# Performance work log

Hardware: AMD Instinct MI355X
Metric: run time of the kernel (lower is better)

Reference implementation:

```python
import jax, jax.numpy as jnp
import numpy as np

B, N, K, UP = 8, 2048, 20, 2
CIN, D, COUT, PH, AH = 256, 64, 128, 64, 256
EPS = 1e-5

def c1(x, W, b):
    # 1x1 Conv1d: x (B,C,N), W (O,C)
    return jnp.einsum('oc,bcn->bon', W, x) + b[None, :, None]

def c2(x, W, b):
    # 1x1 Conv2d: x (B,C,N,K), W (O,C)
    return jnp.einsum('oc,bcnk->bonk', W, x) + b[None, :, None, None]

def bn2(x, g, be):
    # eval-mode BatchNorm2d with running_mean=0, running_var=1
    inv = np.float32(1.0 / np.sqrt(1.0 + EPS))
    return g[None, :, None, None] * x * inv + be[None, :, None, None]

def knn_idx(p, k):
    # p: (B,N,3) -> (B,N,k) indices of k nearest neighbors (incl. self)
    sq = jnp.sum(p * p, -1)
    d = sq[:, :, None] + sq[:, None, :] - 2.0 * jnp.einsum('bnd,bmd->bnm', p, p)
    _, idx = jax.lax.top_k(-d, k)
    return idx

def group(feat, idx):
    # grouping_operation: feat (B,C,N), idx (B,N,k) -> (B,C,N,k)
    return jax.vmap(lambda f, i: f[:, i])(feat, idx)

def setup_inputs() -> dict:
    key = jax.random.key(0)
    ks = jax.random.split(key, 24)
    s = 0.02
    rn = lambda i, shp: jax.random.normal(ks[i], shp, jnp.float32) * s
    return {
        'pos': jax.random.normal(ks[0], (B, 3, N), jnp.float32),
        'key_feat': jax.random.normal(ks[1], (B, CIN, N), jnp.float32),
        'query_feat': jax.random.normal(ks[2], (B, CIN, N), jnp.float32),
        'upfeat': jax.random.normal(ks[3], (B, CIN, N), jnp.float32),
        # mlp_v (MLP_Res): in 2*CIN -> CIN -> CIN with shortcut
        'Wv1': rn(4, (CIN, 2 * CIN)), 'bv1': jnp.zeros(CIN, jnp.float32),
        'Wv2': rn(5, (CIN, CIN)), 'bv2': jnp.zeros(CIN, jnp.float32),
        'Wvs': rn(6, (CIN, 2 * CIN)), 'bvs': jnp.zeros(CIN, jnp.float32),
        # key/query/value/upfeat 1x1 convs CIN -> D
        'Wk': rn(7, (D, CIN)), 'bk': jnp.zeros(D, jnp.float32),
        'Wq': rn(8, (D, CIN)), 'bq': jnp.zeros(D, jnp.float32),
        'Wvv': rn(9, (D, CIN)), 'bvv': jnp.zeros(D, jnp.float32),
        'Wu': rn(10, (D, CIN)), 'bu': jnp.zeros(D, jnp.float32),
        # pos_mlp: 3 -> PH (BN, ReLU) -> D
        'Wp1': rn(11, (PH, 3)), 'bp1': jnp.zeros(PH, jnp.float32),
        'gp1': jnp.ones(PH, jnp.float32), 'betap1': jnp.zeros(PH, jnp.float32),
        'Wp2': rn(12, (D, PH)), 'bp2': jnp.zeros(D, jnp.float32),
        # attn_mlp: D -> AH (BN, ReLU) -> ConvTranspose2d(AH, D, (UP,1), (UP,1))
        'Wa1': rn(13, (AH, D)), 'ba1': jnp.zeros(AH, jnp.float32),
        'ga1': jnp.ones(AH, jnp.float32), 'betaa1': jnp.zeros(AH, jnp.float32),
        'Wt': rn(14, (AH, D, UP)), 'bt': jnp.zeros(D, jnp.float32),
        # conv_end D -> COUT, residual CIN -> COUT
        'Wend': rn(15, (COUT, D)), 'bend': jnp.zeros(COUT, jnp.float32),
        'Wres': rn(16, (COUT, CIN)), 'bres': jnp.zeros(COUT, jnp.float32),
    }

def reference(pos, key_feat, query_feat, upfeat,
              Wv1, bv1, Wv2, bv2, Wvs, bvs,
              Wk, bk, Wq, bq, Wvv, bvv, Wu, bu,
              Wp1, bp1, gp1, betap1, Wp2, bp2,
              Wa1, ba1, ga1, betaa1, Wt, bt,
              Wend, bend, Wres, bres):
    # mlp_v on concat(key, query)
    x = jnp.concatenate([key_feat, query_feat], axis=1)          # (B,2CIN,N)
    value = c1(jax.nn.relu(c1(x, Wv1, bv1)), Wv2, bv2) + c1(x, Wvs, bvs)
    identity = value                                             # (B,CIN,N)
    kf = c1(key_feat, Wk, bk)
    qf = c1(query_feat, Wq, bq)
    vf = c1(value, Wvv, bvv)                                     # (B,D,N)
    idx = knn_idx(pos.transpose(0, 2, 1), K)                     # (B,N,K)
    kg = group(kf, idx)                                          # (B,D,N,K)
    qk_rel = qf[:, :, :, None] - kg
    pos_rel = pos[:, :, :, None] - group(pos, idx)               # (B,3,N,K)
    pos_emb = c2(jax.nn.relu(bn2(c2(pos_rel, Wp1, bp1), gp1, betap1)), Wp2, bp2)
    uf = c1(upfeat, Wu, bu)
    u_rel = uf[:, :, :, None] - group(uf, idx)                   # (B,D,N,K)
    h = jax.nn.relu(bn2(c2(qk_rel + pos_emb + u_rel, Wa1, ba1), ga1, betaa1))  # (B,AH,N,K)
    b = h.shape[0]
    # ConvTranspose2d kernel (UP,1) stride (UP,1): expand N -> N*UP
    att = jnp.einsum('bhnk,hcr->bcnrk', h, Wt).reshape(b, D, N * UP, K) + bt[None, :, None, None]
    att = jax.nn.softmax(att, axis=-1)
    val = group(vf, idx) + pos_emb + u_rel                       # (B,D,N,K)
    val = jnp.repeat(val, UP, axis=2)                            # nearest Upsample (UP,1)
    agg = jnp.sum(att * val, axis=-1)                            # (B,D,N*UP)
    y = c1(agg, Wend, bend)                                      # (B,COUT,N*UP)
    ident = jnp.repeat(c1(identity, Wres, bres), UP, axis=2)     # residual path
    return y + ident
```

## Files before the change

kernel.cpp:

```cpp
#include <hip/hip_runtime.h>
#include <hip/hip_bf16.h>
#include <math.h>

#define BB 8
#define NN 2048
#define KK 20
#define UPF 2
#define CIN 256
#define DD 64
#define COUTN 128
#define PHH 64
#define AHH 256
#define BN_INV 0.9999950000374997f
#define NPB 8

typedef __hip_bfloat16 bf16;
typedef unsigned short u16;
typedef unsigned long long u64;
typedef _Float16 f16;
typedef _Float16 h2   __attribute__((ext_vector_type(2)));
typedef _Float16 f16x4 __attribute__((ext_vector_type(4)));
typedef _Float16 f16x8 __attribute__((ext_vector_type(8)));
typedef float    f32x4 __attribute__((ext_vector_type(4)));

static __device__ __forceinline__ float bf2f(const bf16 v) { return __bfloat162float(v); }
static __device__ __forceinline__ bf16  f2bf(const float v) { return __float2bfloat16(v); }
static __device__ __forceinline__ u16   f2bfu(const float v) {
    return __builtin_bit_cast(u16, __float2bfloat16(v));
}
static __device__ __forceinline__ float lo2f(const unsigned v) { return __builtin_bit_cast(float, v << 16); }
static __device__ __forceinline__ float hi2f(const unsigned v) { return __builtin_bit_cast(float, v & 0xFFFF0000u); }

static __device__ __forceinline__ f32x4 mfma16(const f16x8 a, const f16x8 b, const f32x4 c) {
    return __builtin_amdgcn_mfma_f32_16x16x32_f16(a, b, c, 0, 0, 0);
}
static __device__ __forceinline__ unsigned fmap(const float f) {
    unsigned u = __builtin_bit_cast(unsigned, f);
    return (u >> 31) ? ~u : (u | 0x80000000u);
}

__global__ void sentinel_kernel(float* out) {
    if (threadIdx.x == 0 && blockIdx.x == 0) out[0] = 100.0f;
}

__global__ __launch_bounds__(256) void prep_kernel(
    const float* __restrict__ Wa1, const float* __restrict__ Wp2,
    const float* __restrict__ Wend, const float* __restrict__ Wt,
    const float* __restrict__ Wv1, const float* __restrict__ Wv2,
    const float* __restrict__ Wvs, const float* __restrict__ Wvv,
    const float* __restrict__ Wres,
    const float* __restrict__ Wk, const float* __restrict__ Wq,
    const float* __restrict__ Wu,
    const float* __restrict__ ba1, const float* __restrict__ ga1,
    const float* __restrict__ betaa1,
    f16* __restrict__ Wa1h, f16* __restrict__ Wp2h, f16* __restrict__ Wth,
    float* __restrict__ A1s, float* __restrict__ A1b,
    float* __restrict__ WendT,
    f16* __restrict__ Wv1h, f16* __restrict__ Wv2h, f16* __restrict__ Wvsh,
    f16* __restrict__ Wvvh, f16* __restrict__ Wresh,
    f16* __restrict__ Wkh, f16* __restrict__ Wqh, f16* __restrict__ Wuh) {
    const int t = blockIdx.x * 256 + threadIdx.x;
    if (t < AHH * DD)        Wa1h[t] = (f16)Wa1[t];
    if (t < PHH * DD)        Wp2h[t] = (f16)Wp2[t];
    if (t < COUTN * AHH)     { int cr = t >> 8, hh = t & 255; Wth[t] = (f16)Wt[hh * COUTN + cr]; }
    if (t < AHH) {
        float gsc = ga1[t] * BN_INV;
        A1s[t] = gsc;
        A1b[t] = gsc * ba1[t] + betaa1[t];
    }
    if (t < COUTN * DD)      { int r = t / DD,  c = t % DD;  WendT[c * COUTN + r] = Wend[t]; }
    if (t < CIN * 2 * CIN)   Wv1h[t] = (f16)Wv1[t];
    if (t < CIN * CIN)       Wv2h[t] = (f16)Wv2[t];
    if (t < CIN * 2 * CIN)   Wvsh[t] = (f16)Wvs[t];
    if (t < DD * CIN)        Wvvh[t] = (f16)Wvv[t];
    if (t < COUTN * CIN)     Wresh[t] = (f16)Wres[t];
    if (t < DD * CIN)        Wkh[t]  = (f16)Wk[t];
    if (t < DD * CIN)        Wqh[t]  = (f16)Wq[t];
    if (t < DD * CIN)        Wuh[t]  = (f16)Wu[t];
}

__global__ __launch_bounds__(256) void xpose_kernel(
    const float* __restrict__ key_feat, const float* __restrict__ query_feat,
    const float* __restrict__ upfeat,
    f16* __restrict__ xkqT, f16* __restrict__ xuT) {
    __shared__ float tile[64][65];
    const int b  = blockIdx.x >> 5;
    const int n0 = (blockIdx.x & 31) << 6;
    const int y  = blockIdx.y;
    const int src = y >> 2;
    const int ct  = (y & 3) << 6;
    const int t = threadIdx.x;
    const float* xin = (src == 0) ? key_feat : (src == 1) ? query_feat : upfeat;
    f16* dst; int CT, cb;
    if (src < 2) { dst = xkqT; CT = 512; cb = src * 256 + ct; }
    else         { dst = xuT;  CT = 256; cb = ct; }
    for (int u = t; u < 64 * 64; u += 256) {
        const int c = u >> 6, j = u & 63;
        tile[c][j] = xin[((size_t)b * CIN + ct + c) * NN + n0 + j];
    }
    __syncthreads();
    for (int u = t; u < 64 * 32; u += 256) {
        const int n = u >> 5, c0 = (u & 31) << 1;
        h2 pr; pr.x = (f16)tile[c0][n]; pr.y = (f16)tile[c0 + 1][n];
        ((unsigned*)dst)[(((size_t)b * NN + n0 + n) * CT + cb + c0) >> 1] =
            __builtin_bit_cast(unsigned, pr);
    }
}

__global__ __launch_bounds__(256) void knn_kernel(const float* __restrict__ pos,
                                                  u16* __restrict__ idx_out,
                                                  float* __restrict__ posT) {
    __shared__ float dist[NN];
    __shared__ int   hist[512];
    __shared__ unsigned rmin[4], rmax[4];
    __shared__ u64   cbuf[64];
    __shared__ float q[3];
    __shared__ unsigned minkS;
    __shared__ int   shiftS, jstarS, cntS;
    __shared__ u64   ltbuf[KK];
    __shared__ int   tiebuf[64];
    __shared__ int   ri[4];
    __shared__ unsigned prefS;
    __shared__ int   knS, cnt_lt, cnt_eq;

    const int b = blockIdx.x / NN;
    const int n = blockIdx.x % NN;
    const int t = threadIdx.x;
    const float* pb = pos + (size_t)b * 3 * NN;
    const size_t rowKK = ((size_t)b * NN + n) * KK;

    if (t < 3) {
        float v = pb[(size_t)t * NN + n];
        q[t] = v;
        posT[((size_t)b * NN + n) * 3 + t] = v;
    }
    if (t == 0) { prefS = 0u; knS = KK; cnt_lt = 0; cnt_eq = 0; cntS = 0; jstarS = 0; }
    __syncthreads();
    const float qx = q[0], qy = q[1], qz = q[2];
    const float sqq = __fadd_rn(__fadd_rn(__fmul_rn(qx, qx), __fmul_rn(qy, qy)), __fmul_rn(qz, qz));
    unsigned kmin = 0xFFFFFFFFu, kmax = 0u;
    for (int m = t; m < NN; m += 256) {
        float px = pb[m];
        float py = pb[NN + m];
        float pz = pb[2 * NN + m];
        float sqm = __fadd_rn(__fadd_rn(__fmul_rn(px, px), __fmul_rn(py, py)), __fmul_rn(pz, pz));
        float dt  = __fadd_rn(__fadd_rn(__fmul_rn(qx, px), __fmul_rn(qy, py)), __fmul_rn(qz, pz));
        const float d = __fsub_rn(__fadd_rn(sqq, sqm), __fmul_rn(2.0f, dt));
        dist[m] = d;
        const unsigned key = fmap(d);
        kmin = min(kmin, key);
        kmax = max(kmax, key);
    }
#pragma unroll
    for (int off = 32; off > 0; off >>= 1) {
        kmin = min(kmin, (unsigned)__shfl_down((int)kmin, off, 64));
        kmax = max(kmax, (unsigned)__shfl_down((int)kmax, off, 64));
    }
    if ((t & 63) == 0) { rmin[t >> 6] = kmin; rmax[t >> 6] = kmax; }
    hist[t] = 0; hist[256 + t] = 0;
    __syncthreads();
    if (t == 0) {
        const unsigned mn = min(min(rmin[0], rmin[1]), min(rmin[2], rmin[3]));
        const unsigned mx = max(max(rmax[0], rmax[1]), max(rmax[2], rmax[3]));
        const unsigned range = mx - mn;
        minkS  = mn;
        shiftS = (range >= 256u) ? (24 - __clz((int)range)) : 0;
    }
    __syncthreads();
    const unsigned mink = minkS;
    const int sh = shiftS;

    for (int m = t; m < NN; m += 256) {
        const unsigned bin = (fmap(dist[m]) - mink) >> sh;
        atomicAdd(&hist[((unsigned)(t & 1) << 8) | bin], 1);
    }
    __syncthreads();
    if (t < 64) {
        const int h0  = hist[4 * t + 0] + hist[256 + 4 * t + 0];
        const int h1  = hist[4 * t + 1] + hist[256 + 4 * t + 1];
        const int h2v = hist[4 * t + 2] + hist[256 + 4 * t + 2];
        const int h3  = hist[4 * t + 3] + hist[256 + 4 * t + 3];
        const int lsum = h0 + h1 + h2v + h3;
        int incl = lsum;
#pragma unroll
        for (int off = 1; off < 64; off <<= 1) {
            int v = __shfl_up(incl, off, 64);
            if (t >= off) incl += v;
        }
        const int excl = incl - lsum;
        if (excl < KK && excl + lsum >= KK) {
            int bsel;
            if      (excl + h0 >= KK)            bsel = 0;
            else if (excl + h0 + h1 >= KK)       bsel = 1;
            else if (excl + h0 + h1 + h2v >= KK) bsel = 2;
            else                                 bsel = 3;
            jstarS = 4 * t + bsel;
        }
    }
    __syncthreads();
    const unsigned jstar = (unsigned)jstarS;

    for (int m = t; m < NN; m += 256) {
        const unsigned key = fmap(dist[m]);
        if (((key - mink) >> sh) <= jstar) {
            const int p = atomicAdd(&cntS, 1);
            if (p < 64) cbuf[p] = ((u64)key << 32) | (unsigned)m;
        }
    }
    __syncthreads();
    const int total = cntS;

    if (total <= 64) {
        if (t < 64) {
            u64 v = (t < total) ? cbuf[t] : 0xFFFFFFFFFFFFFFFFull;
            int rank = 0;
#pragma unroll 16
            for (int j = 0; j < 64; ++j) {
                const u64 o = (u64)__shfl((long long)v, j, 64);
                if (o < v) ++rank;
            }
            if (t < total && rank < KK) idx_out[rowKK + rank] = (u16)(v & 0xFFFFu);
        }
        return;
    }

    for (int pass = 0; pass < 4; ++pass) {
        const int shift = 24 - 8 * pass;
        const unsigned pm = (pass == 0) ? 0u : (0xFFFFFFFFu << (32 - 8 * pass));
        hist[t] = 0;
        __syncthreads();
        const unsigned pref = prefS;
        const int kn = knS;
        for (int m = t; m < NN; m += 256) {
            unsigned key = fmap(dist[m]);
            if ((key & pm) == pref)
                atomicAdd(&hist[(key >> shift) & 255], 1);
        }
        __syncthreads();
        if (t < 64) {
            const int h0 = hist[4 * t + 0], h1 = hist[4 * t + 1];
            const int h2v = hist[4 * t + 2], h3 = hist[4 * t + 3];
            const int lsum = h0 + h1 + h2v + h3;
            int incl = lsum;
#pragma unroll
            for (int off = 1; off < 64; off <<= 1) {
                int v = __shfl_up(incl, off, 64);
                if (t >= off) incl += v;
            }
            const int excl = incl - lsum;
            if (excl < kn && excl + lsum >= kn) {
                int bsel, cb;
                if      (excl + h0 >= kn)            { bsel = 0; cb = excl; }
                else if (excl + h0 + h1 >= kn)       { bsel = 1; cb = excl + h0; }
                else if (excl + h0 + h1 + h2v >= kn) { bsel = 2; cb = excl + h0 + h1; }
                else                                 { bsel = 3; cb = excl + h0 + h1 + h2v; }
                knS = kn - cb;
                prefS = pref | ((unsigned)(4 * t + bsel) << shift);
            }
        }
        __syncthreads();
    }

    const unsigned T = prefS;
    for (int m = t; m < NN; m += 256) {
        unsigned key = fmap(dist[m]);
        if (key < T) {
            int p = atomicAdd(&cnt_lt, 1);
            ltbuf[p] = ((u64)key << 32) | (unsigned)m;
        } else if (key == T) {
            int p = atomicAdd(&cnt_eq, 1);
            if (p < 64) tiebuf[p] = m;
        }
    }
    __syncthreads();
    const int nlt = cnt_lt, neq_need = knS, ceq = cnt_eq;

    if (t < 64) {
        u64 v = (t < nlt) ? ltbuf[t] : 0xFFFFFFFFFFFFFFFFull;
        int rank = 0;
#pragma unroll
        for (int j = 0; j < KK; ++j) {
            const u64 o = (u64)__shfl((long long)v, j, 64);
            if (o < v) ++rank;
        }
        if (t < nlt) idx_out[rowKK + rank] = (u16)(v & 0xFFFFu);
    }
    if (ceq <= 64) {
        if (t < 64) {
            int ti = (t < ceq) ? tiebuf[t] : 0x7FFFFFFF;
            int rk = 0;
            for (int j = 0; j < 64; ++j) {
                const int o = __shfl(ti, j, 64);
                if (o < ti) ++rk;
            }
            if (t < ceq && rk < neq_need) idx_out[rowKK + nlt + rk] = (u16)ti;
        }
    } else {
        for (int iter = 0; iter < neq_need; ++iter) {
            int bi = NN;
            for (int m = t; m < NN; m += 256)
                if (fmap(dist[m]) == T && m < bi) bi = m;
            for (int off = 32; off > 0; off >>= 1) {
                int i2 = __shfl_down(bi, off, 64);
                bi = min(bi, i2);
            }
            if ((t & 63) == 0) ri[t >> 6] = bi;
            __syncthreads();
            if (t == 0) {
                int i0 = min(min(ri[0], ri[1]), min(ri[2], ri[3]));
                idx_out[rowKK + nlt + iter] = (u16)i0;
                dist[i0] = 3.4e38f;
            }
            __syncthreads();
        }
    }
}

__global__ __launch_bounds__(256) void value_mfma(
    const f16* __restrict__ xkqT,
    const f16* __restrict__ Wv1h, const float* __restrict__ bv1,
    const f16* __restrict__ Wv2h, const float* __restrict__ bv2,
    const f16* __restrict__ Wvsh, const float* __restrict__ bvs,
    const f16* __restrict__ Wvvh, const float* __restrict__ bvv,
    const f16* __restrict__ Wresh, const float* __restrict__ bres,
    bf16* __restrict__ vf_ws, bf16* __restrict__ resid_ws) {
    __shared__ __align__(16) char hv[32 * 512];
    const int b  = blockIdx.x >> 6;
    const int n0 = (blockIdx.x & 63) << 5;
    const int t = threadIdx.x;
    const int w = t >> 6, l = t & 63, g = l >> 4, li = l & 15;
    const f16* xb = xkqT + ((size_t)b * NN + n0) * 512;
    const f32x4 zero4 = {0.f, 0.f, 0.f, 0.f};

    f32x4 a1[4][2];
#pragma unroll
    for (int mt = 0; mt < 4; ++mt) { a1[mt][0] = zero4; a1[mt][1] = zero4; }
    for (int ks = 0; ks < 16; ++ks) {
        f16x8 bx0 = *(const f16x8*)(xb + (size_t)li * 512 + ks * 32 + g * 8);
        f16x8 bx1 = *(const f16x8*)(xb + (size_t)(16 + li) * 512 + ks * 32 + g * 8);
#pragma unroll
        for (int mt = 0; mt < 4; ++mt) {
            const f16x8 af = *(const f16x8*)(Wv1h + (size_t)(w * 64 + mt * 16 + li) * 512 + ks * 32 + g * 8);
            a1[mt][0] = mfma16(af, bx0, a1[mt][0]);
            a1[mt][1] = mfma16(af, bx1, a1[mt][1]);
        }
    }
#pragma unroll
    for (int mt = 0; mt < 4; ++mt) {
        const int ch0 = w * 64 + mt * 16 + g * 4;
        const float4 b4 = *(const float4*)(bv1 + ch0);
#pragma unroll
        for (int nt = 0; nt < 2; ++nt) {
            const int n = nt * 16 + li;
            f16x4 px;
            px.x = (f16)fmaxf(a1[mt][nt][0] + b4.x, 0.f);
            px.y = (f16)fmaxf(a1[mt][nt][1] + b4.y, 0.f);
            px.z = (f16)fmaxf(a1[mt][nt][2] + b4.z, 0.f);
            px.w = (f16)fmaxf(a1[mt][nt][3] + b4.w, 0.f);
            *(f16x4*)(hv + n * 512 + ((ch0 * 2) ^ ((n & 7) << 4))) = px;
        }
    }
    __syncthreads();

    f32x4 a2[4][2];
#pragma unroll
    for (int mt = 0; mt < 4; ++mt) { a2[mt][0] = zero4; a2[mt][1] = zero4; }
    for (int ks = 0; ks < 8; ++ks) {
        f16x8 bh[2];
#pragma unroll
        for (int nt = 0; nt < 2; ++nt) {
            const int n = nt * 16 + li;
            bh[nt] = *(const f16x8*)(hv + n * 512 + ((ks * 64 + g * 16) ^ ((n & 7) << 4)));
        }
#pragma unroll
        for (int mt = 0; mt < 4; ++mt) {
            const f16x8 af = *(const f16x8*)(Wv2h + (size_t)(w * 64 + mt * 16 + li) * 256 + ks * 32 + g * 8);
            a2[mt][0] = mfma16(af, bh[0], a2[mt][0]);
            a2[mt][1] = mfma16(af, bh[1], a2[mt][1]);
        }
    }
    for (int ks = 0; ks < 16; ++ks) {
        f16x8 bx0 = *(const f16x8*)(xb + (size_t)li * 512 + ks * 32 + g * 8);
        f16x8 bx1 = *(const f16x8*)(xb + (size_t)(16 + li) * 512 + ks * 32 + g * 8);
#pragma unroll
        for (int mt = 0; mt < 4; ++mt) {
            const f16x8 af = *(const f16x8*)(Wvsh + (size_t)(w * 64 + mt * 16 + li) * 512 + ks * 32 + g * 8);
            a2[mt][0] = mfma16(af, bx0, a2[mt][0]);
            a2[mt][1] = mfma16(af, bx1, a2[mt][1]);
        }
    }
    __syncthreads();
#pragma unroll
    for (int mt = 0; mt < 4; ++mt) {
        const int ch0 = w * 64 + mt * 16 + g * 4;
        const float4 c4a = *(const float4*)(bv2 + ch0);
        const float4 c4b = *(const float4*)(bvs + ch0);
#pragma unroll
        for (int nt = 0; nt < 2; ++nt) {
            const int n = nt * 16 + li;
            f16x4 px;
            px.x = (f16)(a2[mt][nt][0] + c4a.x + c4b.x);
            px.y = (f16)(a2[mt][nt][1] + c4a.y + c4b.y);
            px.z = (f16)(a2[mt][nt][2] + c4a.z + c4b.z);
            px.w = (f16)(a2[mt][nt][3] + c4a.w + c4b.w);
            *(f16x4*)(hv + n * 512 + ((ch0 * 2) ^ ((n & 7) << 4))) = px;
        }
    }
    __syncthreads();

    f32x4 av[2] = {zero4, zero4};
    f32x4 ar[2][2];
    ar[0][0] = zero4; ar[0][1] = zero4; ar[1][0] = zero4; ar[1][1] = zero4;
    for (int ks = 0; ks < 8; ++ks) {
        f16x8 bh[2];
#pragma unroll
        for (int nt = 0; nt < 2; ++nt) {
            const int n = nt * 16 + li;
            bh[nt] = *(const f16x8*)(hv + n * 512 + ((ks * 64 + g * 16) ^ ((n & 7) << 4)));
        }
        const f16x8 afv = *(const f16x8*)(Wvvh + (size_t)(w * 16 + li) * 256 + ks * 32 + g * 8);
        av[0] = mfma16(afv, bh[0], av[0]);
        av[1] = mfma16(afv, bh[1], av[1]);
#pragma unroll
        for (int rt = 0; rt < 2; ++rt) {
            const f16x8 afr = *(const f16x8*)(Wresh + (size_t)((w * 2 + rt) * 16 + li) * 256 + ks * 32 + g * 8);
            ar[rt][0] = mfma16(afr, bh[0], ar[rt][0]);
            ar[rt][1] = mfma16(afr, bh[1], ar[rt][1]);
        }
    }
    {
        const int ch0 = w * 16 + g * 4;
        const float4 bb = *(const float4*)(bvv + ch0);
#pragma unroll
        for (int nt = 0; nt < 2; ++nt) {
            const int n = nt * 16 + li;
            ushort4 pk;
            pk.x = f2bfu(av[nt][0] + bb.x);
            pk.y = f2bfu(av[nt][1] + bb.y);
            pk.z = f2bfu(av[nt][2] + bb.z);
            pk.w = f2bfu(av[nt][3] + bb.w);
            *(ushort4*)((char*)vf_ws + (((size_t)b * NN + n0 + n) * DD + ch0) * 2) = pk;
        }
    }
#pragma unroll
    for (int rt = 0; rt < 2; ++rt) {
        const int ch0 = (w * 2 + rt) * 16 + g * 4;
        const float4 bb = *(const float4*)(bres + ch0);
#pragma unroll
        for (int nt = 0; nt < 2; ++nt) {
            const int n = nt * 16 + li;
            ushort4 pk;
            pk.x = f2bfu(ar[rt][nt][0] + bb.x);
            pk.y = f2bfu(ar[rt][nt][1] + bb.y);
            pk.z = f2bfu(ar[rt][nt][2] + bb.z);
            pk.w = f2bfu(ar[rt][nt][3] + bb.w);
            *(ushort4*)((char*)resid_ws + (((size_t)b * NN + n0 + n) * COUTN + ch0) * 2) = pk;
        }
    }
}

__global__ __launch_bounds__(256) void proj_mfma(
    const f16* __restrict__ xkqT, const f16* __restrict__ xuT,
    const f16* __restrict__ Wkh, const float* __restrict__ bk,
    const f16* __restrict__ Wqh, const float* __restrict__ bq,
    const f16* __restrict__ Wuh, const float* __restrict__ bu,
    bf16* __restrict__ kf, bf16* __restrict__ qf, bf16* __restrict__ uf) {
    const int b  = blockIdx.x >> 6;
    const int n0 = (blockIdx.x & 63) << 5;
    const int t = threadIdx.x;
    const int w = t >> 6, l = t & 63, g = l >> 4, li = l & 15;
    if (w == 3) return;
    const f16* xb; int stride; const f16* W; const float* bias; bf16* out;
    if (w == 0)      { xb = xkqT + ((size_t)b * NN + n0) * 512;       stride = 512; W = Wkh; bias = bk; out = kf; }
    else if (w == 1) { xb = xkqT + ((size_t)b * NN + n0) * 512 + 256; stride = 512; W = Wqh; bias = bq; out = qf; }
    else             { xb = xuT + ((size_t)b * NN + n0) * 256;        stride = 256; W = Wuh; bias = bu; out = uf; }
    const f32x4 zero4 = {0.f, 0.f, 0.f, 0.f};
    f32x4 acc[4][2];
#pragma unroll
    for (int mt = 0; mt < 4; ++mt) { acc[mt][0] = zero4; acc[mt][1] = zero4; }
    for (int ks = 0; ks < 8; ++ks) {
        f16x8 bx0 = *(const f16x8*)(xb + (size_t)li * stride + ks * 32 + g * 8);
        f16x8 bx1 = *(const f16x8*)(xb + (size_t)(16 + li) * stride + ks * 32 + g * 8);
#pragma unroll
        for (int mt = 0; mt < 4; ++mt) {
            const f16x8 af = *(const f16x8*)(W + (size_t)(mt * 16 + li) * 256 + ks * 32 + g * 8);
            acc[mt][0] = mfma16(af, bx0, acc[mt][0]);
            acc[mt][1] = mfma16(af, bx1, acc[mt][1]);
        }
    }
#pragma unroll
    for (int mt = 0; mt < 4; ++mt) {
        const int ch0 = mt * 16 + g * 4;
        const float4 bb = *(const float4*)(bias + ch0);
#pragma unroll
        for (int nt = 0; nt < 2; ++nt) {
            const int n = nt * 16 + li;
            ushort4 pk;
            pk.x = f2bfu(acc[mt][nt][0] + bb.x);
            pk.y = f2bfu(acc[mt][nt][1] + bb.y);
            pk.z = f2bfu(acc[mt][nt][2] + bb.z);
            pk.w = f2bfu(acc[mt][nt][3] + bb.w);
            *(ushort4*)((char*)out + (((size_t)b * NN + n0 + n) * DD + ch0) * 2) = pk;
        }
    }
}

__global__ __launch_bounds__(512, 4) void attn_fused(
    const float* __restrict__ posT, const u16* __restrict__ idx_ws,
    const bf16* __restrict__ kf_ws, const bf16* __restrict__ qf_ws,
    const bf16* __restrict__ uf_ws, const bf16* __restrict__ vf_ws,
    const bf16* __restrict__ resid_ws,
    const float* __restrict__ Wp1, const float* __restrict__ bp1,
    const float* __restrict__ gp1, const float* __restrict__ betap1,
    const f16* __restrict__ Wp2h, const float* __restrict__ bp2,
    const f16* __restrict__ Wa1h, const float* __restrict__ A1s,
    const float* __restrict__ A1b, const f16* __restrict__ Wth,
    const float* __restrict__ WendT, const float* __restrict__ bend,
    float* __restrict__ out) {
    __shared__ __align__(16) char pool[61440];
    f16*  ph16 = (f16*)(pool);
    f16*  S16  = (f16*)(pool);
    f16*  L16T = (f16*)(pool);
    f16*  peh  = (f16*)(pool + 20480);
    char* Hl   = pool + 20480;
    f16*  V16  = (f16*)(pool + 40960);
    __shared__ int   nidx[8 * KK];
    __shared__ float prel[8 * KK][3];
    __shared__ float qcol[NPB][64], ucol[NPB][64];
    __shared__ float aggl[NPB][COUTN];

    const int b  = blockIdx.x >> 8;
    const int n0 = (blockIdx.x & 255) << 3;
    const int t = threadIdx.x;
    const int w = t >> 6, l = t & 63, g = l >> 4, li = l & 15;
    const int m4 = w & 3, nh = w >> 2;
    const size_t row0 = (size_t)b * NN + n0;
    const f32x4 zero4 = {0.f, 0.f, 0.f, 0.f};

    if (t < 8 * KK) nidx[t] = (int)idx_ws[row0 * KK + t];
    __syncthreads();

    {
        const int n = t >> 6, c = t & 63;
        qcol[n][c] = bf2f(qf_ws[(row0 + n) * DD + c]);
        ucol[n][c] = bf2f(uf_ws[(row0 + n) * DD + c]);
    }
    if (t < 480) {
        const int r = t / 3, d = t - r * 3;
        const int n = r / KK;
        prel[r][d] = posT[(row0 + n) * 3 + d] - posT[((size_t)b * NN + nidx[r]) * 3 + d];
    }
    __syncthreads();

    for (int u = t; u < 160 * 32; u += 512) {
        const int r = u >> 5, c0 = (u & 31) << 1;
        float a0 = Wp1[c0 * 3 + 0] * prel[r][0] + Wp1[c0 * 3 + 1] * prel[r][1]
                 + Wp1[c0 * 3 + 2] * prel[r][2] + bp1[c0];
        float a1 = Wp1[c0 * 3 + 3] * prel[r][0] + Wp1[c0 * 3 + 4] * prel[r][1]
                 + Wp1[c0 * 3 + 5] * prel[r][2] + bp1[c0 + 1];
        a0 = gp1[c0] * a0 * BN_INV + betap1[c0];
        a1 = gp1[c0 + 1] * a1 * BN_INV + betap1[c0 + 1];
        h2 pr; pr.x = (f16)fmaxf(a0, 0.f); pr.y = (f16)fmaxf(a1, 0.f);
        *(unsigned*)((char*)ph16 + (r * 128 + ((c0 * 2) ^ ((r & 7) << 4)))) =
            __builtin_bit_cast(unsigned, pr);
    }
    __syncthreads();

    {
        f32x4 d[5];
#pragma unroll
        for (int j = 0; j < 5; ++j) d[j] = zero4;
#pragma unroll
        for (int ks = 0; ks < 2; ++ks) {
            const f16x8 af = *(const f16x8*)(Wp2h + (m4 * 16 + li) * 64 + ks * 32 + g * 8);
#pragma unroll
            for (int j = 0; j < 5; ++j) {
                const int r = (nh * 5 + j) * 16 + li;
                const f16x8 bf = *(const f16x8*)((const char*)ph16 +
                                  (r * 128 + ((ks * 64 + g * 16) ^ ((r & 7) << 4))));
                d[j] = mfma16(af, bf, d[j]);
            }
        }
        const int ch0 = m4 * 16 + g * 4;
        const float4 b4 = *(const float4*)(bp2 + ch0);
#pragma unroll
        for (int j = 0; j < 5; ++j) {
            const int r = (nh * 5 + j) * 16 + li;
            f16x4 pk;
            pk.x = (f16)(d[j][0] + b4.x);
            pk.y = (f16)(d[j][1] + b4.y);
            pk.z = (f16)(d[j][2] + b4.z);
            pk.w = (f16)(d[j][3] + b4.w);
            *(f16x4*)((char*)peh + (r * 128 + ((ch0 * 2) ^ ((r & 7) << 4)))) = pk;
        }
    }
    __syncthreads();

    for (int u = t; u < 160 * 32; u += 512) {
        const int r = u >> 5, c0 = (u & 31) << 1;
        const int n = r / KK;
        const size_t nb2 = (((size_t)b * NN + nidx[r]) * DD + c0) * 2;
        const unsigned kq = *(const unsigned*)((const char*)kf_ws + nb2);
        const unsigned uq = *(const unsigned*)((const char*)uf_ws + nb2);
        const unsigned vq = *(const unsigned*)((const char*)vf_ws + nb2);
        const unsigned pw = *(const unsigned*)((const char*)peh +
                              (r * 128 + ((c0 * 2) ^ ((r & 7) << 4))));
        const h2 pp = __builtin_bit_cast(h2, pw);
        const float add0 = ucol[n][c0] + (float)pp.x;
        const float add1 = ucol[n][c0 + 1] + (float)pp.y;
        const float gb0 = -(lo2f(kq) + lo2f(uq));
        const float gb1 = -(hi2f(kq) + hi2f(uq));
        const float vb0 = lo2f(vq) - lo2f(uq);
        const float vb1 = hi2f(vq) - hi2f(uq);
        h2 s; s.x = (f16)(gb0 + qcol[n][c0] + add0); s.y = (f16)(gb1 + qcol[n][c0 + 1] + add1);
        h2 v; v.x = (f16)(vb0 + add0);               v.y = (f16)(vb1 + add1);
        const int sw = (c0 * 2) ^ ((r & 7) << 4);
        *(unsigned*)((char*)S16 + (r * 128 + sw)) = __builtin_bit_cast(unsigned, s);
        *(unsigned*)((char*)V16 + (r * 128 + sw)) = __builtin_bit_cast(unsigned, v);
    }
    __syncthreads();

    f32x4 acc2[10];
#pragma unroll
    for (int j = 0; j < 10; ++j) acc2[j] = zero4;

    for (int c4 = 0; c4 < 4; ++c4) {
        const int hrb = c4 * 64 + m4 * 16;
        f32x4 d1[5];
#pragma unroll
        for (int j = 0; j < 5; ++j) d1[j] = zero4;
#pragma unroll
        for (int ks = 0; ks < 2; ++ks) {
            const f16x8 af = *(const f16x8*)(Wa1h + (hrb + li) * 64 + ks * 32 + g * 8);
#pragma unroll
            for (int j = 0; j < 5; ++j) {
                const int r = (nh * 5 + j) * 16 + li;
                const f16x8 sfv = *(const f16x8*)((const char*)S16 +
                                   (r * 128 + ((ks * 64 + g * 16) ^ ((r & 7) << 4))));
                d1[j] = mfma16(af, sfv, d1[j]);
            }
        }
        const float4 as4 = *(const float4*)(A1s + hrb + g * 4);
        const float4 ab4 = *(const float4*)(A1b + hrb + g * 4);
        __syncthreads();
#pragma unroll
        for (int j = 0; j < 5; ++j) {
            const int col = (nh * 5 + j) * 16 + li;
            const int ch0 = m4 * 16 + g * 4;
            f16x4 pk;
            pk.x = (f16)fmaxf(as4.x * d1[j][0] + ab4.x, 0.f);
            pk.y = (f16)fmaxf(as4.y * d1[j][1] + ab4.y, 0.f);
            pk.z = (f16)fmaxf(as4.z * d1[j][2] + ab4.z, 0.f);
            pk.w = (f16)fmaxf(as4.w * d1[j][3] + ab4.w, 0.f);
            *(f16x4*)(Hl + col * 128 + ((ch0 * 2) ^ ((col & 7) << 4))) = pk;
        }
        __syncthreads();
#pragma unroll
        for (int ks2 = 0; ks2 < 2; ++ks2) {
            const f16x8 bf = *(const f16x8*)(Wth + (size_t)(w * 16 + li) * AHH + c4 * 64 + ks2 * 32 + g * 8);
#pragma unroll
            for (int nt = 0; nt < 10; ++nt) {
                const int col = nt * 16 + li;
                const f16x8 ha = *(const f16x8*)(Hl + col * 128 + ((ks2 * 64 + g * 16) ^ ((col & 7) << 4)));
                acc2[nt] = mfma16(ha, bf, acc2[nt]);
            }
        }
    }
    __syncthreads();

#pragma unroll
    for (int nt = 0; nt < 10; ++nt) {
        const f32x4 d = acc2[nt];
#pragma unroll
        for (int j = 0; j < 4; ++j) {
            const int row = nt * 16 + g * 4 + j;
            *(f16*)((char*)L16T + (row * 256 + (((w * 16 + li) * 2) ^ ((row & 3) << 5)))) =
                (f16)d[j];
        }
    }
    __syncthreads();

    {
        const int cr = t & 127, c = cr >> 1;
        const int nbase = (t >> 7) * 2;
        for (int p = 0; p < 2; ++p) {
            const int n = nbase + p;
            float lv[20];
#pragma unroll
            for (int k = 0; k < 20; ++k) {
                const int row = n * KK + k;
                lv[k] = (float)*(const f16*)((const char*)L16T +
                          (row * 256 + ((cr * 2) ^ ((row & 3) << 5))));
            }
            float m = lv[0];
#pragma unroll
            for (int k = 1; k < 20; ++k) m = fmaxf(m, lv[k]);
            float s = 0.f, a = 0.f;
#pragma unroll
            for (int k = 0; k < 20; ++k) {
                const float e = expf(lv[k] - m);
                s += e;
                const int r = n * KK + k;
                const float vv = (float)*(const f16*)((const char*)V16 +
                                   (r * 128 + ((c * 2) ^ ((r & 7) << 4))));
                a += e * vv;
            }
            aggl[n][cr] = a / s;
        }
    }
    __syncthreads();

    {
        const int o = t & 127, np = t >> 7;
        const int na = 2 * np, nb = 2 * np + 1;
        float a0r0 = 0.f, a0r1 = 0.f, a1r0 = 0.f, a1r1 = 0.f;
        for (int cc = 0; cc < DD; ++cc) {
            const float wv = WendT[cc * COUTN + o];
            a0r0 += wv * aggl[na][cc * 2];
            a0r1 += wv * aggl[na][cc * 2 + 1];
            a1r0 += wv * aggl[nb][cc * 2];
            a1r1 += wv * aggl[nb][cc * 2 + 1];
        }
        const float be = bend[o];
        const float r0 = bf2f(resid_ws[(row0 + na) * COUTN + o]);
        const float r1 = bf2f(resid_ws[(row0 + nb) * COUTN + o]);
        float4 ov;
        ov.x = a0r0 + be + r0; ov.y = a0r1 + be + r0;
        ov.z = a1r0 + be + r1; ov.w = a1r1 + be + r1;
        *(float4*)(out + (size_t)b * COUTN * (NN * UPF) + (size_t)o * (NN * UPF) + 2 * n0 + 4 * np) = ov;
    }
}

extern "C" void kernel_launch(void* const* d_in, const int* in_sizes, int n_in,
                              void* d_out, int out_size, void* d_ws, size_t ws_size,
                              hipStream_t stream) {
    const float* pos        = (const float*)d_in[0];
    const float* key_feat   = (const float*)d_in[1];
    const float* query_feat = (const float*)d_in[2];
    const float* upfeat     = (const float*)d_in[3];
    const float* Wv1 = (const float*)d_in[4];
    const float* bv1 = (const float*)d_in[5];
    const float* Wv2 = (const float*)d_in[6];
    const float* bv2 = (const float*)d_in[7];
    const float* Wvs = (const float*)d_in[8];
    const float* bvs = (const float*)d_in[9];
    const float* Wk  = (const float*)d_in[10];
    const float* bk  = (const float*)d_in[11];
    const float* Wq  = (const float*)d_in[12];
    const float* bq  = (const float*)d_in[13];
    const float* Wvv = (const float*)d_in[14];
    const float* bvv = (const float*)d_in[15];
    const float* Wu  = (const float*)d_in[16];
    const float* bu  = (const float*)d_in[17];
    const float* Wp1 = (const float*)d_in[18];
    const float* bp1 = (const float*)d_in[19];
    const float* gp1 = (const float*)d_in[20];
    const float* betap1 = (const float*)d_in[21];
    const float* Wp2 = (const float*)d_in[22];
    const float* bp2 = (const float*)d_in[23];
    const float* Wa1 = (const float*)d_in[24];
    const float* ba1 = (const float*)d_in[25];
    const float* ga1 = (const float*)d_in[26];
    const float* betaa1 = (const float*)d_in[27];
    const float* Wt   = (const float*)d_in[28];
    const float* bt   = (const float*)d_in[29];
    const float* Wend = (const float*)d_in[30];
    const float* bend = (const float*)d_in[31];
    const float* Wres = (const float*)d_in[32];
    const float* bres = (const float*)d_in[33];
    float* out = (float*)d_out;
    (void)out_size; (void)bt;

    const bool sizes_ok = (n_in >= 34)
        && (in_sizes[0] == BB * 3 * NN)
        && (in_sizes[1] == BB * CIN * NN)
        && (in_sizes[4] == CIN * 2 * CIN)
        && (in_sizes[28] == AHH * DD * UPF)
        && (in_sizes[32] == COUTN * CIN);

    size_t off = 0;
    auto take = [&](size_t bytes) { size_t o = off; off = (off + bytes + 255) & ~(size_t)255; return o; };
    const size_t off_posT  = take((size_t)BB * NN * 3 * sizeof(float));
    const size_t off_idx   = take((size_t)BB * NN * KK * sizeof(u16));
    const size_t off_vf    = take((size_t)BB * NN * DD * sizeof(bf16));
    const size_t off_kf    = take((size_t)BB * NN * DD * sizeof(bf16));
    const size_t off_qf    = take((size_t)BB * NN * DD * sizeof(bf16));
    const size_t off_uf    = take((size_t)BB * NN * DD * sizeof(bf16));
    const size_t off_resid = take((size_t)BB * NN * COUTN * sizeof(bf16));
    const size_t off_wa1h  = take((size_t)AHH * DD * sizeof(f16));
    const size_t off_wp2h  = take((size_t)PHH * DD * sizeof(f16));
    const size_t off_wth   = take((size_t)COUTN * AHH * sizeof(f16));
    const size_t off_a1s   = take((size_t)AHH * sizeof(float));
    const size_t off_a1b   = take((size_t)AHH * sizeof(float));
    const size_t off_wendt = take((size_t)COUTN * DD * sizeof(float));
    const size_t off_wv1h  = take((size_t)CIN * 2 * CIN * sizeof(f16));
    const size_t off_wv2h  = take((size_t)CIN * CIN * sizeof(f16));
    const size_t off_wvsh  = take((size_t)CIN * 2 * CIN * sizeof(f16));
    const size_t off_wvvh  = take((size_t)DD * CIN * sizeof(f16));
    const size_t off_wresh = take((size_t)COUTN * CIN * sizeof(f16));
    const size_t off_wkh   = take((size_t)DD * CIN * sizeof(f16));
    const size_t off_wqh   = take((size_t)DD * CIN * sizeof(f16));
    const size_t off_wuh   = take((size_t)DD * CIN * sizeof(f16));
    const size_t off_xkq   = take((size_t)BB * NN * 512 * sizeof(f16));
    const size_t off_xu    = take((size_t)BB * NN * 256 * sizeof(f16));
    const size_t NEED = off;

    if (!sizes_ok) return;
    if (ws_size < NEED) {
        sentinel_kernel<<<1, 64, 0, stream>>>(out);
        return;
    }

    char* ws = (char*)d_ws;
    float* posT_ws  = (float*)(ws + off_posT);
    u16*   idx_ws   = (u16*)(ws + off_idx);
    bf16*  vf_ws    = (bf16*)(ws + off_vf);
    bf16*  kf_ws    = (bf16*)(ws + off_kf);
    bf16*  qf_ws    = (bf16*)(ws + off_qf);
    bf16*  uf_ws    = (bf16*)(ws + off_uf);
    bf16*  resid_ws = (bf16*)(ws + off_resid);
    f16*   Wa1h_ws  = (f16*)(ws + off_wa1h);
    f16*   Wp2h_ws  = (f16*)(ws + off_wp2h);
    f16*   Wth_ws   = (f16*)(ws + off_wth);
    float* A1s_ws   = (float*)(ws + off_a1s);
    float* A1b_ws   = (float*)(ws + off_a1b);
    float* WendT_ws = (float*)(ws + off_wendt);
    f16*   Wv1h_ws  = (f16*)(ws + off_wv1h);
    f16*   Wv2h_ws  = (f16*)(ws + off_wv2h);
    f16*   Wvsh_ws  = (f16*)(ws + off_wvsh);
    f16*   Wvvh_ws  = (f16*)(ws + off_wvvh);
    f16*   Wresh_ws = (f16*)(ws + off_wresh);
    f16*   Wkh_ws   = (f16*)(ws + off_wkh);
    f16*   Wqh_ws   = (f16*)(ws + off_wqh);
    f16*   Wuh_ws   = (f16*)(ws + off_wuh);
    f16*   xkqT_ws  = (f16*)(ws + off_xkq);
    f16*   xuT_ws   = (f16*)(ws + off_xu);

    prep_kernel<<<(CIN * 2 * CIN + 255) / 256, 256, 0, stream>>>(
        Wa1, Wp2, Wend, Wt, Wv1, Wv2, Wvs, Wvv, Wres, Wk, Wq, Wu,
        ba1, ga1, betaa1,
        Wa1h_ws, Wp2h_ws, Wth_ws, A1s_ws, A1b_ws, WendT_ws,
        Wv1h_ws, Wv2h_ws, Wvsh_ws, Wvvh_ws, Wresh_ws, Wkh_ws, Wqh_ws, Wuh_ws);
    xpose_kernel<<<dim3(BB * (NN / 64), 12), 256, 0, stream>>>(
        key_feat, query_feat, upfeat, xkqT_ws, xuT_ws);
    knn_kernel<<<BB * NN, 256, 0, stream>>>(pos, idx_ws, posT_ws);
    value_mfma<<<BB * (NN / 32), 256, 0, stream>>>(xkqT_ws,
        Wv1h_ws, bv1, Wv2h_ws, bv2, Wvsh_ws, bvs, Wvvh_ws, bvv, Wresh_ws, bres,
        vf_ws, resid_ws);
    proj_mfma<<<BB * (NN / 32), 256, 0, stream>>>(xkqT_ws, xuT_ws,
        Wkh_ws, bk, Wqh_ws, bq, Wuh_ws, bu, kf_ws, qf_ws, uf_ws);
    attn_fused<<<BB * (NN / NPB), 512, 0, stream>>>(posT_ws, idx_ws,
        kf_ws, qf_ws, uf_ws, vf_ws, resid_ws,
        Wp1, bp1, gp1, betap1, Wp2h_ws, bp2,
        Wa1h_ws, A1s_ws, A1b_ws, Wth_ws, WendT_ws, bend, out);
}
```

Before: 447.7 us.

## Fuse K/Q/U projections into value kernel and use MFMA for final conv

Removes the separate proj_mfma launch by computing the key, query and upfeat projections inside value_mfma, reusing the already-loaded xkqT fragments for K and Q. The final Wend 1x1 conv in attn_fused moves from a scalar FP32 loop over LDS to a 16x16 f16 MFMA, with aggregated values stored as swizzled f16 in shared memory and the weight converted to f16 in prep. It also swaps expf for __expf in the softmax. Costs are lower precision in the output conv, more register pressure in value_mfma, and scalar (non-float4) output stores.

```diff
diff --git a/kernel.cpp b/kernel.cpp
--- a/kernel.cpp
+++ b/kernel.cpp
@@ -55,7 +55,7 @@
     const float* __restrict__ betaa1,
     f16* __restrict__ Wa1h, f16* __restrict__ Wp2h, f16* __restrict__ Wth,
     float* __restrict__ A1s, float* __restrict__ A1b,
-    float* __restrict__ WendT,
+    f16* __restrict__ Wendh,
     f16* __restrict__ Wv1h, f16* __restrict__ Wv2h, f16* __restrict__ Wvsh,
     f16* __restrict__ Wvvh, f16* __restrict__ Wresh,
     f16* __restrict__ Wkh, f16* __restrict__ Wqh, f16* __restrict__ Wuh) {
@@ -68,7 +68,7 @@
         A1s[t] = gsc;
         A1b[t] = gsc * ba1[t] + betaa1[t];
     }
-    if (t < COUTN * DD)      { int r = t / DD,  c = t % DD;  WendT[c * COUTN + r] = Wend[t]; }
+    if (t < COUTN * DD)      Wendh[t] = (f16)Wend[t];
     if (t < CIN * 2 * CIN)   Wv1h[t] = (f16)Wv1[t];
     if (t < CIN * CIN)       Wv2h[t] = (f16)Wv2[t];
     if (t < CIN * 2 * CIN)   Wvsh[t] = (f16)Wvs[t];
@@ -317,13 +317,17 @@
 }
 
 __global__ __launch_bounds__(256) void value_mfma(
-    const f16* __restrict__ xkqT,
+    const f16* __restrict__ xkqT, const f16* __restrict__ xuT,
     const f16* __restrict__ Wv1h, const float* __restrict__ bv1,
     const f16* __restrict__ Wv2h, const float* __restrict__ bv2,
     const f16* __restrict__ Wvsh, const float* __restrict__ bvs,
     const f16* __restrict__ Wvvh, const float* __restrict__ bvv,
     const f16* __restrict__ Wresh, const float* __restrict__ bres,
-    bf16* __restrict__ vf_ws, bf16* __restrict__ resid_ws) {
+    const f16* __restrict__ Wkh, const float* __restrict__ bk,
+    const f16* __restrict__ Wqh, const float* __restrict__ bq,
+    const f16* __restrict__ Wuh, const float* __restrict__ bu,
+    bf16* __restrict__ vf_ws, bf16* __restrict__ resid_ws,
+    bf16* __restrict__ kf, bf16* __restrict__ qf, bf16* __restrict__ uf) {
     __shared__ __align__(16) char hv[32 * 512];
     const int b  = blockIdx.x >> 6;
     const int n0 = (blockIdx.x & 63) << 5;
@@ -333,6 +337,7 @@
     const f32x4 zero4 = {0.f, 0.f, 0.f, 0.f};
 
     f32x4 a1[4][2];
+    f32x4 ak[2] = {zero4, zero4}, aq[2] = {zero4, zero4};
 #pragma unroll
     for (int mt = 0; mt < 4; ++mt) { a1[mt][0] = zero4; a1[mt][1] = zero4; }
     for (int ks = 0; ks < 16; ++ks) {
@@ -343,6 +348,26 @@
             const f16x8 af = *(const f16x8*)(Wv1h + (size_t)(w * 64 + mt * 16 + li) * 512 + ks * 32 + g * 8);
             a1[mt][0] = mfma16(af, bx0, a1[mt][0]);
             a1[mt][1] = mfma16(af, bx1, a1[mt][1]);
+        }
+        if (ks < 8) {
+            const f16x8 afk = *(const f16x8*)(Wkh + (size_t)(w * 16 + li) * 256 + ks * 32 + g * 8);
+            ak[0] = mfma16(afk, bx0, ak[0]);
+            ak[1] = mfma16(afk, bx1, ak[1]);
+        } else {
+            const f16x8 afq = *(const f16x8*)(Wqh + (size_t)(w * 16 + li) * 256 + (ks - 8) * 32 + g * 8);
+            aq[0] = mfma16(afq, bx0, aq[0]);
+            aq[1] = mfma16(afq, bx1, aq[1]);
+        }
+    }
+    f32x4 au[2] = {zero4, zero4};
+    {
+        const f16* xub = xuT + ((size_t)b * NN + n0) * 256;
+        for (int ks = 0; ks < 8; ++ks) {
+            f16x8 bu0 = *(const f16x8*)(xub + (size_t)li * 256 + ks * 32 + g * 8);
+            f16x8 bu1 = *(const f16x8*)(xub + (size_t)(16 + li) * 256 + ks * 32 + g * 8);
+            const f16x8 af = *(const f16x8*)(Wuh + (size_t)(w * 16 + li) * 256 + ks * 32 + g * 8);
+            au[0] = mfma16(af, bu0, au[0]);
+            au[1] = mfma16(af, bu1, au[1]);
         }
     }
 #pragma unroll
@@ -360,6 +385,27 @@
             *(f16x4*)(hv + n * 512 + ((ch0 * 2) ^ ((n & 7) << 4))) = px;
         }
     }
+    {
+        const int ch0 = w * 16 + g * 4;
+        const float4 bk4 = *(const float4*)(bk + ch0);
+        const float4 bq4 = *(const float4*)(bq + ch0);
+        const float4 bu4 = *(const float4*)(bu + ch0);
+#pragma unroll
+        for (int nt = 0; nt < 2; ++nt) {
+            const int n = nt * 16 + li;
+            const size_t base = ((size_t)b * NN + n0 + n) * DD + ch0;
+            ushort4 pk, pq, pu;
+            pk.x = f2bfu(ak[nt][0] + bk4.x); pk.y = f2bfu(ak[nt][1] + bk4.y);
+            pk.z = f2bfu(ak[nt][2] + bk4.z); pk.w = f2bfu(ak[nt][3] + bk4.w);
+            pq.x = f2bfu(aq[nt][0] + bq4.x); pq.y = f2bfu(aq[nt][1] + bq4.y);
+            pq.z = f2bfu(aq[nt][2] + bq4.z); pq.w = f2bfu(aq[nt][3] + bq4.w);
+            pu.x = f2bfu(au[nt][0] + bu4.x); pu.y = f2bfu(au[nt][1] + bu4.y);
+            pu.z = f2bfu(au[nt][2] + bu4.z); pu.w = f2bfu(au[nt][3] + bu4.w);
+            *(ushort4*)((char*)kf + base * 2) = pk;
+            *(ushort4*)((char*)qf + base * 2) = pq;
+            *(ushort4*)((char*)uf + base * 2) = pu;
+        }
+    }
     __syncthreads();
 
     f32x4 a2[4][2];
@@ -455,52 +501,6 @@
             pk.z = f2bfu(ar[rt][nt][2] + bb.z);
             pk.w = f2bfu(ar[rt][nt][3] + bb.w);
             *(ushort4*)((char*)resid_ws + (((size_t)b * NN + n0 + n) * COUTN + ch0) * 2) = pk;
-        }
-    }
-}
-
-__global__ __launch_bounds__(256) void proj_mfma(
-    const f16* __restrict__ xkqT, const f16* __restrict__ xuT,
-    const f16* __restrict__ Wkh, const float* __restrict__ bk,
-    const f16* __restrict__ Wqh, const float* __restrict__ bq,
-    const f16* __restrict__ Wuh, const float* __restrict__ bu,
-    bf16* __restrict__ kf, bf16* __restrict__ qf, bf16* __restrict__ uf) {
-    const int b  = blockIdx.x >> 6;
-    const int n0 = (blockIdx.x & 63) << 5;
-    const int t = threadIdx.x;
-    const int w = t >> 6, l = t & 63, g = l >> 4, li = l & 15;
-    if (w == 3) return;
-    const f16* xb; int stride; const f16* W; const float* bias; bf16* out;
-    if (w == 0)      { xb = xkqT + ((size_t)b * NN + n0) * 512;       stride = 512; W = Wkh; bias = bk; out = kf; }
-    else if (w == 1) { xb = xkqT + ((size_t)b * NN + n0) * 512 + 256; stride = 512; W = Wqh; bias = bq; out = qf; }
-    else             { xb = xuT + ((size_t)b * NN + n0) * 256;        stride = 256; W = Wuh; bias = bu; out = uf; }
-    const f32x4 zero4 = {0.f, 0.f, 0.f, 0.f};
-    f32x4 acc[4][2];
-#pragma unroll
-    for (int mt = 0; mt < 4; ++mt) { acc[mt][0] = zero4; acc[mt][1] = zero4; }
-    for (int ks = 0; ks < 8; ++ks) {
-        f16x8 bx0 = *(const f16x8*)(xb + (size_t)li * stride + ks * 32 + g * 8);
-        f16x8 bx1 = *(const f16x8*)(xb + (size_t)(16 + li) * stride + ks * 32 + g * 8);
-#pragma unroll
-        for (int mt = 0; mt < 4; ++mt) {
-            const f16x8 af = *(const f16x8*)(W + (size_t)(mt * 16 + li) * 256 + ks * 32 + g * 8);
-            acc[mt][0] = mfma16(af, bx0, acc[mt][0]);
-            acc[mt][1] = mfma16(af, bx1, acc[mt][1]);
-        }
-    }
-#pragma unroll
-    for (int mt = 0; mt < 4; ++mt) {
-        const int ch0 = mt * 16 + g * 4;
-        const float4 bb = *(const float4*)(bias + ch0);
-#pragma unroll
-        for (int nt = 0; nt < 2; ++nt) {
-            const int n = nt * 16 + li;
-            ushort4 pk;
-            pk.x = f2bfu(acc[mt][nt][0] + bb.x);
-            pk.y = f2bfu(acc[mt][nt][1] + bb.y);
-            pk.z = f2bfu(acc[mt][nt][2] + bb.z);
-            pk.w = f2bfu(acc[mt][nt][3] + bb.w);
-            *(ushort4*)((char*)out + (((size_t)b * NN + n0 + n) * DD + ch0) * 2) = pk;
         }
     }
 }
@@ -515,7 +515,7 @@
     const f16* __restrict__ Wp2h, const float* __restrict__ bp2,
     const f16* __restrict__ Wa1h, const float* __restrict__ A1s,
     const float* __restrict__ A1b, const f16* __restrict__ Wth,
-    const float* __restrict__ WendT, const float* __restrict__ bend,
+    const f16* __restrict__ Wendh, const float* __restrict__ bend,
     float* __restrict__ out) {
     __shared__ __align__(16) char pool[61440];
     f16*  ph16 = (f16*)(pool);
@@ -524,10 +524,10 @@
     f16*  peh  = (f16*)(pool + 20480);
     char* Hl   = pool + 20480;
     f16*  V16  = (f16*)(pool + 40960);
+    __shared__ __align__(16) f16 aggf[16 * 64];
     __shared__ int   nidx[8 * KK];
     __shared__ float prel[8 * KK][3];
     __shared__ float qcol[NPB][64], ucol[NPB][64];
-    __shared__ float aggl[NPB][COUTN];
 
     const int b  = blockIdx.x >> 8;
     const int n0 = (blockIdx.x & 255) << 3;
@@ -681,7 +681,7 @@
     __syncthreads();
 
     {
-        const int cr = t & 127, c = cr >> 1;
+        const int cr = t & 127, c = cr >> 1, rr = cr & 1;
         const int nbase = (t >> 7) * 2;
         for (int p = 0; p < 2; ++p) {
             const int n = nbase + p;
@@ -698,36 +698,36 @@
             float s = 0.f, a = 0.f;
 #pragma unroll
             for (int k = 0; k < 20; ++k) {
-                const float e = expf(lv[k] - m);
+                const float e = __expf(lv[k] - m);
                 s += e;
                 const int r = n * KK + k;
                 const float vv = (float)*(const f16*)((const char*)V16 +
                                    (r * 128 + ((c * 2) ^ ((r & 7) << 4))));
                 a += e * vv;
             }
-            aggl[n][cr] = a / s;
+            const int arow = n * 2 + rr;
+            *(f16*)((char*)aggf + (arow * 128 + ((c * 2) ^ ((arow & 7) << 4)))) = (f16)(a / s);
         }
     }
     __syncthreads();
 
     {
-        const int o = t & 127, np = t >> 7;
-        const int na = 2 * np, nb = 2 * np + 1;
-        float a0r0 = 0.f, a0r1 = 0.f, a1r0 = 0.f, a1r1 = 0.f;
-        for (int cc = 0; cc < DD; ++cc) {
-            const float wv = WendT[cc * COUTN + o];
-            a0r0 += wv * aggl[na][cc * 2];
-            a0r1 += wv * aggl[na][cc * 2 + 1];
-            a1r0 += wv * aggl[nb][cc * 2];
-            a1r1 += wv * aggl[nb][cc * 2 + 1];
-        }
-        const float be = bend[o];
-        const float r0 = bf2f(resid_ws[(row0 + na) * COUTN + o]);
-        const float r1 = bf2f(resid_ws[(row0 + nb) * COUTN + o]);
-        float4 ov;
-        ov.x = a0r0 + be + r0; ov.y = a0r1 + be + r0;
-        ov.z = a1r0 + be + r1; ov.w = a1r1 + be + r1;
-        *(float4*)(out + (size_t)b * COUTN * (NN * UPF) + (size_t)o * (NN * UPF) + 2 * n0 + 4 * np) = ov;
+        f32x4 dc = zero4;
+#pragma unroll
+        for (int ks = 0; ks < 2; ++ks) {
+            const f16x8 af = *(const f16x8*)(Wendh + (size_t)(w * 16 + li) * 64 + ks * 32 + g * 8);
+            const f16x8 bfr = *(const f16x8*)((const char*)aggf +
+                               (li * 128 + (((ks * 32 + g * 8) * 2) ^ ((li & 7) << 4))));
+            dc = mfma16(af, bfr, dc);
+        }
+        const int nloc = li >> 1;
+#pragma unroll
+        for (int j = 0; j < 4; ++j) {
+            const int o = w * 16 + g * 4 + j;
+            const float rv = bf2f(resid_ws[(row0 + nloc) * COUTN + o]);
+            out[(size_t)b * COUTN * (NN * UPF) + (size_t)o * (NN * UPF) + 2 * n0 + li] =
+                dc[j] + bend[o] + rv;
+        }
     }
 }
 
@@ -792,7 +792,7 @@
     const size_t off_wth   = take((size_t)COUTN * AHH * sizeof(f16));
     const size_t off_a1s   = take((size_t)AHH * sizeof(float));
     const size_t off_a1b   = take((size_t)AHH * sizeof(float));
-    const size_t off_wendt = take((size_t)COUTN * DD * sizeof(float));
+    const size_t off_wendh = take((size_t)COUTN * DD * sizeof(f16));
     const size_t off_wv1h  = take((size_t)CIN * 2 * CIN * sizeof(f16));
     const size_t off_wv2h  = take((size_t)CIN * CIN * sizeof(f16));
     const size_t off_wvsh  = take((size_t)CIN * 2 * CIN * sizeof(f16));
@@ -824,7 +824,7 @@
     f16*   Wth_ws   = (f16*)(ws + off_wth);
     float* A1s_ws   = (float*)(ws + off_a1s);
     float* A1b_ws   = (float*)(ws + off_a1b);
-    float* WendT_ws = (float*)(ws + off_wendt);
+    f16*   Wendh_ws = (f16*)(ws + off_wendh);
     f16*   Wv1h_ws  = (f16*)(ws + off_wv1h);
     f16*   Wv2h_ws  = (f16*)(ws + off_wv2h);
     f16*   Wvsh_ws  = (f16*)(ws + off_wvsh);
@@ -839,18 +839,17 @@
     prep_kernel<<<(CIN * 2 * CIN + 255) / 256, 256, 0, stream>>>(
         Wa1, Wp2, Wend, Wt, Wv1, Wv2, Wvs, Wvv, Wres, Wk, Wq, Wu,
         ba1, ga1, betaa1,
-        Wa1h_ws, Wp2h_ws, Wth_ws, A1s_ws, A1b_ws, WendT_ws,
+        Wa1h_ws, Wp2h_ws, Wth_ws, A1s_ws, A1b_ws, Wendh_ws,
         Wv1h_ws, Wv2h_ws, Wvsh_ws, Wvvh_ws, Wresh_ws, Wkh_ws, Wqh_ws, Wuh_ws);
     xpose_kernel<<<dim3(BB * (NN / 64), 12), 256, 0, stream>>>(
         key_feat, query_feat, upfeat, xkqT_ws, xuT_ws);
     knn_kernel<<<BB * NN, 256, 0, stream>>>(pos, idx_ws, posT_ws);
-    value_mfma<<<BB * (NN / 32), 256, 0, stream>>>(xkqT_ws,
+    value_mfma<<<BB * (NN / 32), 256, 0, stream>>>(xkqT_ws, xuT_ws,
         Wv1h_ws, bv1, Wv2h_ws, bv2, Wvsh_ws, bvs, Wvvh_ws, bvv, Wresh_ws, bres,
-        vf_ws, resid_ws);
-    proj_mfma<<<BB * (NN / 32), 256, 0, stream>>>(xkqT_ws, xuT_ws,
-        Wkh_ws, bk, Wqh_ws, bq, Wuh_ws, bu, kf_ws, qf_ws, uf_ws);
+        Wkh_ws, bk, Wqh_ws, bq, Wuh_ws, bu,
+        vf_ws, resid_ws, kf_ws, qf_ws, uf_ws);
     attn_fused<<<BB * (NN / NPB), 512, 0, stream>>>(posT_ws, idx_ws,
         kf_ws, qf_ws, uf_ws, vf_ws, resid_ws,
         Wp1, bp1, gp1, betap1, Wp2h_ws, bp2,
-        Wa1h_ws, A1s_ws, A1b_ws, Wth_ws, WendT_ws, bend, out);
-}
+        Wa1h_ws, A1s_ws, A1b_ws, Wth_ws, Wendh_ws, bend, out);
+}
```

Result: faster. 426.7 us (-4.7%).
